# Optimization experiments

Hardware: AMD Instinct MI355X
Metric: run time of the kernel (lower is better)

## Reference

```python
import jax, jax.numpy as jnp
import numpy as np

H = 16          # hidden_size
L = 24          # num_layers
LEN_TRAIN = 96
LEN_PRED = 48
B = 256         # leading dim of input (acts as TIME axis for the LSTMs, see notes)


def setup_inputs() -> dict:
    key = jax.random.key(0)
    ks = jax.random.split(key, 16)
    s = 1.0 / np.sqrt(H)  # PyTorch LSTM/Linear init scale
    u = lambda k, shp: jax.random.uniform(k, shp, jnp.float32, -s, s)
    return {
        "x": jax.random.normal(ks[0], (B, 1, LEN_TRAIN), jnp.float32),
        # lstm1: layer0 input_size=1, layers 1..23 input_size=2H
        "W_ih0_1": u(ks[1], (2, 4 * H, 1)),
        "W_ih_1": u(ks[2], (L - 1, 2, 4 * H, 2 * H)),
        "W_hh_1": u(ks[3], (L, 2, 4 * H, H)),
        "b_ih_1": u(ks[4], (L, 2, 4 * H)),
        "b_hh_1": u(ks[5], (L, 2, 4 * H)),
        # lstm2: all layers input_size=2H
        "W_ih_2": u(ks[6], (L, 2, 4 * H, 2 * H)),
        "W_hh_2": u(ks[7], (L, 2, 4 * H, H)),
        "b_ih_2": u(ks[8], (L, 2, 4 * H)),
        "b_hh_2": u(ks[9], (L, 2, 4 * H)),
        "fc1_w": u(ks[10], (1000, 2 * LEN_PRED * H)),
        "fc1_b": u(ks[11], (1000,)),
        "fc2_w": u(ks[12], (LEN_PRED, 1000)),
        "fc2_b": u(ks[13], (LEN_PRED,)),
    }


def _lstm_dir(x, Wih, Whh, bih, bhh, reverse):
    # x: (T, N, in). Precompute input-gate GEMM over whole sequence.
    xg = jnp.einsum("tni,gi->tng", x, Wih) + bih + bhh  # (T, N, 4H)

    def step(carry, g_in):
        h, c = carry
        g = g_in + h @ Whh.T
        i, f, gg, o = jnp.split(g, 4, axis=-1)  # PyTorch gate order i,f,g,o
        c = jax.nn.sigmoid(f) * c + jax.nn.sigmoid(i) * jnp.tanh(gg)
        h = jax.nn.sigmoid(o) * jnp.tanh(c)
        return (h, c), h

    N = x.shape[1]
    init = (jnp.zeros((N, H), x.dtype), jnp.zeros((N, H), x.dtype))
    _, hs = jax.lax.scan(step, init, xg, reverse=reverse)
    return hs  # (T, N, H), in original time order


def _bilstm_stack(x, Wih_per_layer, Whh, bih, bhh):
    for l in range(Whh.shape[0]):
        Wih = Wih_per_layer[l]
        fwd = _lstm_dir(x, Wih[0], Whh[l, 0], bih[l, 0], bhh[l, 0], False)
        bwd = _lstm_dir(x, Wih[1], Whh[l, 1], bih[l, 1], bhh[l, 1], True)
        x = jnp.concatenate([fwd, bwd], axis=-1)  # (T, N, 2H)
    return x


def reference(x, W_ih0_1, W_ih_1, W_hh_1, b_ih_1, b_hh_1,
              W_ih_2, W_hh_2, b_ih_2, b_hh_2,
              fc1_w, fc1_b, fc2_w, fc2_b):
    xp = jnp.transpose(x, (0, 2, 1))  # (B, 96, 1); dim0 is the LSTM time axis (batch_first=False quirk)
    wih1 = [W_ih0_1] + [W_ih_1[i] for i in range(L - 1)]
    h = _bilstm_stack(xp, wih1, W_hh_1, b_ih_1, b_hh_1)      # (B, 96, 2H)
    x1 = h[:, -LEN_PRED:, :]                                  # (B, 48, 2H)
    wih2 = [W_ih_2[i] for i in range(L)]
    h2 = _bilstm_stack(x1, wih2, W_hh_2, b_ih_2, b_hh_2)      # (B, 48, 2H)
    z = h2 + x1
    flat = z.reshape(z.shape[0], -1)                          # (B, 1536)
    y = jax.nn.relu(flat @ fc1_w.T + fc1_b) @ fc2_w.T + fc2_b # (B, 48)
    return jnp.transpose(y.reshape(y.shape[0], LEN_PRED, 1), (0, 2, 1))  # (B, 1, 48)
```

## Files before the change

### kernel.cpp

```cpp
#include <hip/hip_runtime.h>


template <int SEL>
__device__ __forceinline__ float quad_bcast(float v) {
  return __int_as_float(__builtin_amdgcn_update_dpp(
      0, __float_as_int(v), SEL * 0x55, 0xF, 0xF, true));
}

__global__ __launch_bounds__(512, 2) void lstm_fused(
    const float* __restrict__ x, const float* __restrict__ W_ih0_1,
    const float* __restrict__ W_ih_1, const float* __restrict__ W_hh_1,
    const float* __restrict__ b_ih_1, const float* __restrict__ b_hh_1,
    const float* __restrict__ W_ih_2, const float* __restrict__ W_hh_2,
    const float* __restrict__ b_ih_2, const float* __restrict__ b_hh_2,
    float* __restrict__ x1out, float* __restrict__ h2out) {
  __shared__ float xgF[256 * 64];
  __shared__ float xgB[256 * 64];

  const int tid = threadIdx.x;
  const int lane = tid & 63;
  const int w = tid >> 6;
  const int np = blockIdx.x;
  const int nglob = 48 + np;

  const bool rec = (w == 0) || (w == 5);
  const int d = (w == 5) ? 1 : 0;
  const bool ovl = (w == 2) || (w == 3) || (w == 6) || (w == 7);
  const int ovlIdx = (w & 1) | ((w >> 2) << 1);
  const int widx = (w < 5) ? (w - 1) : (w - 2);

  {
    const int dd = w >> 2;
    const int wv = w & 3;
    float* xg = dd ? xgB : xgF;
    const float bias = b_ih_1[dd * 64 + lane] + b_hh_1[dd * 64 + lane];
    const float wih0 = W_ih0_1[dd * 64 + lane];
    const int xvb = __float_as_int(x[(size_t)(wv * 64 + lane) * 96 + nglob]);
    for (int ti = 0; ti < 64; ++ti) {
      const float xs = __int_as_float(__builtin_amdgcn_readlane(xvb, ti));
      xg[(wv * 64 + ti) * 64 + lane] = fmaf(wih0, xs, bias);
    }
  }

  int g = 0, r = 0;
  float s_ = 0.f, m_ = 0.f, b_ = 0.f;
  float whn[16];
  if (rec) {
    g = lane & 3;
    r = g * 16 + (lane >> 2);
    s_ = (g == 2) ? 2.885390082f : -1.442695041f;
    m_ = (g == 2) ? -2.0f : 1.0f;
    b_ = (g == 2) ? 1.0f : 0.0f;
    const float* W0 = W_hh_1 + (size_t)d * 1024 + (size_t)r * 16;
#pragma unroll
    for (int k = 0; k < 16; ++k) whn[k] = W0[k];
  }
  __syncthreads();

  for (int L = 0; L < 48; ++L) {
    float whh[16];
    if (rec) {
#pragma unroll
      for (int k = 0; k < 16; ++k) whh[k] = whn[k];
      const int M = (L < 47) ? (L + 1) : 47;
      const float* Wn = ((M < 24) ? (W_hh_1 + (size_t)M * 2048)
                                  : (W_hh_2 + (size_t)(M - 24) * 2048)) +
                        (size_t)d * 1024 + (size_t)r * 16;
#pragma unroll
      for (int k = 0; k < 16; ++k) whn[k] = Wn[k];
    }

    float wf[32], wb[32], bf = 0.f, bb = 0.f;
    if (!rec) {
      const int M = (L < 47) ? (L + 1) : 47;
      const float* WihP;
      const float* bihP;
      const float* bhhP;
      if (M < 24) {
        WihP = W_ih_1 + (size_t)(M - 1) * 4096;
        bihP = b_ih_1 + (size_t)M * 128;
        bhhP = b_hh_1 + (size_t)M * 128;
      } else {
        WihP = W_ih_2 + (size_t)(M - 24) * 4096;
        bihP = b_ih_2 + (size_t)(M - 24) * 128;
        bhhP = b_hh_2 + (size_t)(M - 24) * 128;
      }
      bf = bihP[lane] + bhhP[lane];
      bb = bihP[64 + lane] + bhhP[64 + lane];
      const float4* pf =
          reinterpret_cast<const float4*>(WihP + (size_t)lane * 32);
      const float4* pb =
          reinterpret_cast<const float4*>(WihP + 2048 + (size_t)lane * 32);
#pragma unroll
      for (int q = 0; q < 8; ++q) {
        const float4 a = pf[q];
        wf[4 * q + 0] = a.x;
        wf[4 * q + 1] = a.y;
        wf[4 * q + 2] = a.z;
        wf[4 * q + 3] = a.w;
        const float4 b = pb[q];
        wb[4 * q + 0] = b.x;
        wb[4 * q + 1] = b.y;
        wb[4 * q + 2] = b.z;
        wb[4 * q + 3] = b.w;
      }
    }

    auto compute_row = [&](int t, const float4 (&F)[4], const float4 (&Bv)[4]) {
      float f0 = bf, f1 = 0.f, f2 = 0.f, f3 = 0.f;
      float g0 = bb, g1 = 0.f, g2 = 0.f, g3 = 0.f;
#pragma unroll
      for (int q = 0; q < 4; ++q) {
        const float4 a = F[q];
        f0 = fmaf(wf[4 * q + 0], a.x, f0);
        f1 = fmaf(wf[4 * q + 1], a.y, f1);
        f2 = fmaf(wf[4 * q + 2], a.z, f2);
        f3 = fmaf(wf[4 * q + 3], a.w, f3);
        g0 = fmaf(wb[4 * q + 0], a.x, g0);
        g1 = fmaf(wb[4 * q + 1], a.y, g1);
        g2 = fmaf(wb[4 * q + 2], a.z, g2);
        g3 = fmaf(wb[4 * q + 3], a.w, g3);
        const float4 b = Bv[q];
        f0 = fmaf(wf[16 + 4 * q + 0], b.x, f0);
        f1 = fmaf(wf[16 + 4 * q + 1], b.y, f1);
        f2 = fmaf(wf[16 + 4 * q + 2], b.z, f2);
        f3 = fmaf(wf[16 + 4 * q + 3], b.w, f3);
        g0 = fmaf(wb[16 + 4 * q + 0], b.x, g0);
        g1 = fmaf(wb[16 + 4 * q + 1], b.y, g1);
        g2 = fmaf(wb[16 + 4 * q + 2], b.z, g2);
        g3 = fmaf(wb[16 + 4 * q + 3], b.w, g3);
      }
      xgF[t * 64 + lane] = (f0 + f1) + (f2 + f3);
      xgB[t * 64 + lane] = (g0 + g1) + (g2 + g3);
    };

    auto phaseA_rows = [&](int t0, int cnt) {
      float4 af[4], ab4[4], nf[4], nb[4];
      {
        const float4* qf = reinterpret_cast<const float4*>(&xgF[t0 * 64]);
        const float4* qb = reinterpret_cast<const float4*>(&xgB[t0 * 64]);
#pragma unroll
        for (int q = 0; q < 4; ++q) {
          af[q] = qf[q];
          ab4[q] = qb[q];
        }
      }
      for (int i = 0; i < cnt; i += 2) {
        const int t = t0 + i;
        {
          const float4* qf =
              reinterpret_cast<const float4*>(&xgF[(t + 1) * 64]);
          const float4* qb =
              reinterpret_cast<const float4*>(&xgB[(t + 1) * 64]);
#pragma unroll
          for (int q = 0; q < 4; ++q) {
            nf[q] = qf[q];
            nb[q] = qb[q];
          }
        }
        compute_row(t, af, ab4);
        if (i + 2 < cnt) {
          const float4* qf =
              reinterpret_cast<const float4*>(&xgF[(t + 2) * 64]);
          const float4* qb =
              reinterpret_cast<const float4*>(&xgB[(t + 2) * 64]);
#pragma unroll
          for (int q = 0; q < 4; ++q) {
            af[q] = qf[q];
            ab4[q] = qb[q];
          }
        }
        compute_row(t + 1, nf, nb);
      }
    };

    float hs[16];
    float c = 0.f;
    int t = d ? 255 : 0;
    const int dt = d ? -1 : 1;
    float cur0 = 0.f, cur1 = 0.f;
    float* xg = d ? xgB : xgF;

#define LSTM_STEP(CUR, TT)                                                  \
  {                                                                         \
    float a0 = (CUR), a1 = 0.f, a2 = 0.f, a3 = 0.f;                         \
    _Pragma("unroll") for (int k = 0; k < 16; k += 4) {                     \
      a0 = fmaf(whh[k + 0], hs[k + 0], a0);                                 \
      a1 = fmaf(whh[k + 1], hs[k + 1], a1);                                 \
      a2 = fmaf(whh[k + 2], hs[k + 2], a2);                                 \
      a3 = fmaf(whh[k + 3], hs[k + 3], a3);                                 \
    }                                                                       \
    const float gv = (a0 + a1) + (a2 + a3);                                 \
    const float e = __builtin_amdgcn_exp2f(s_ * gv);                        \
    const float v = fmaf(m_, __builtin_amdgcn_rcpf(1.0f + e), b_);          \
    const float si = quad_bcast<0>(v);                                      \
    const float sf = quad_bcast<1>(v);                                      \
    const float tg = quad_bcast<2>(v);                                      \
    const float so = quad_bcast<3>(v);                                      \
    c = fmaf(sf, c, si * tg);                                               \
    const float e2 = __builtin_amdgcn_exp2f(2.885390082f * c);              \
    const float th = fmaf(-2.0f, __builtin_amdgcn_rcpf(1.0f + e2), 1.0f);   \
    const float h = so * th;                                                \
    xg[(TT)*64 + r] = h;  \
    const int hb = __float_as_int(h);                                       \
    _Pragma("unroll") for (int k = 0; k < 16; ++k) hs[k] =                  \
        __int_as_float(__builtin_amdgcn_readlane(hb, 4 * k));               \
  }

    auto run_steps = [&](int nsteps) {
      for (int tt = 0; tt < nsteps; tt += 2) {
        const float nx0 = xg[((t + 2 * dt) & 255) * 64 + r];
        LSTM_STEP(cur0, t)
        const float nx1 = xg[((t + 3 * dt) & 255) * 64 + r];
        LSTM_STEP(cur1, t + dt)
        cur0 = nx0;
        cur1 = nx1;
        t += 2 * dt;
      }
    };

    if (rec) {
#pragma unroll
      for (int k = 0; k < 16; ++k) hs[k] = 0.f;
      cur0 = xg[t * 64 + r];
      cur1 = xg[(t + dt) * 64 + r];
      run_steps(192);
    }
    __syncthreads();

    if (rec) {
      __builtin_amdgcn_s_setprio(1);
      run_steps(64);
      __builtin_amdgcn_s_setprio(0);
    } else if (ovl && L != 23 && L != 47) {
      phaseA_rows(64 + ovlIdx * 32, 32);
    }
#undef LSTM_STEP
    __syncthreads();

    if (L == 23 || L == 47) {
      float* dst = (L == 23) ? x1out : h2out;
#pragma unroll
      for (int p = 0; p < 4; ++p) {
        const int gi = p * 512 + tid;
        const int tt = gi >> 3;
        const int cc = gi & 7;
        const float* src =
            (cc < 4) ? &xgF[tt * 64 + cc * 4] : &xgB[tt * 64 + (cc - 4) * 4];
        const float4 v = *reinterpret_cast<const float4*>(src);
        *reinterpret_cast<float4*>(dst + ((size_t)tt * 48 + np) * 32 +
                                   cc * 4) = v;
      }
      if (L == 47) break;
      __syncthreads();
      if (!rec) {
        const int t0 = (widx < 4) ? widx * 44 : 176 + (widx - 4) * 40;
        phaseA_rows(t0, (widx < 4) ? 44 : 40);
      }
    } else {
      if (!rec) {
        const int half = widx / 3;
        const int k3 = widx - half * 3;
        phaseA_rows(half * 192 + k3 * 22, (k3 == 2) ? 20 : 22);
      }
    }
    __syncthreads();
  }
}

__global__ __launch_bounds__(256) void fc1_kernel(
    const float* __restrict__ h2, const float* __restrict__ x1b,
    const float* __restrict__ w1, const float* __restrict__ b1,
    float* __restrict__ y1) {
  __shared__ float Zs[16][68];
  __shared__ float Ws[16][68];
  const int tid = threadIdx.x;
  const int m0 = blockIdx.x * 64;
  const int b0 = blockIdx.y * 64;
  const int rr = tid >> 2;
  const int c4 = (tid & 3) * 4;
  const int tx = tid & 15, ty = tid >> 4;

  float acc[4][4];
#pragma unroll
  for (int i = 0; i < 4; ++i)
#pragma unroll
    for (int jj = 0; jj < 4; ++jj) acc[i][jj] = 0.f;

  const bool wvalid = (m0 + rr) < 1000;
  const float* zr = h2 + (size_t)(b0 + rr) * 1536 + c4;
  const float* zr2 = x1b + (size_t)(b0 + rr) * 1536 + c4;
  const float* wr = w1 + (size_t)(m0 + rr) * 1536 + c4;

  float4 za = *reinterpret_cast<const float4*>(zr);
  float4 zb = *reinterpret_cast<const float4*>(zr2);
  float4 wv = wvalid ? *reinterpret_cast<const float4*>(wr)
                     : make_float4(0.f, 0.f, 0.f, 0.f);

  for (int k0 = 0; k0 < 1536; k0 += 16) {
    Zs[c4 + 0][rr] = za.x + zb.x;
    Zs[c4 + 1][rr] = za.y + zb.y;
    Zs[c4 + 2][rr] = za.z + zb.z;
    Zs[c4 + 3][rr] = za.w + zb.w;
    Ws[c4 + 0][rr] = wv.x;
    Ws[c4 + 1][rr] = wv.y;
    Ws[c4 + 2][rr] = wv.z;
    Ws[c4 + 3][rr] = wv.w;
    if (k0 + 16 < 1536) {
      za = *reinterpret_cast<const float4*>(zr + k0 + 16);
      zb = *reinterpret_cast<const float4*>(zr2 + k0 + 16);
      if (wvalid) wv = *reinterpret_cast<const float4*>(wr + k0 + 16);
    }
    __syncthreads();
#pragma unroll
    for (int kk = 0; kk < 16; ++kk) {
      const float4 av = *reinterpret_cast<const float4*>(&Zs[kk][ty * 4]);
      const float4 bv = *reinterpret_cast<const float4*>(&Ws[kk][tx * 4]);
      const float a_[4] = {av.x, av.y, av.z, av.w};
      const float b_[4] = {bv.x, bv.y, bv.z, bv.w};
#pragma unroll
      for (int i = 0; i < 4; ++i)
#pragma unroll
        for (int jj = 0; jj < 4; ++jj)
          acc[i][jj] = fmaf(a_[i], b_[jj], acc[i][jj]);
    }
    __syncthreads();
  }
#pragma unroll
  for (int i = 0; i < 4; ++i) {
    const int b = b0 + ty * 4 + i;
#pragma unroll
    for (int jj = 0; jj < 4; ++jj) {
      const int m = m0 + tx * 4 + jj;
      if (m < 1000) {
        float vo = acc[i][jj] + b1[m];
        y1[(size_t)b * 1000 + m] = vo > 0.f ? vo : 0.f;
      }
    }
  }
}

__global__ __launch_bounds__(64) void fc2_kernel(
    const float* __restrict__ y1, const float* __restrict__ w2,
    const float* __restrict__ b2, float* __restrict__ out) {
  __shared__ float ys[1000];
  const int b = blockIdx.x;
  for (int k = threadIdx.x; k < 1000; k += 64) ys[k] = y1[(size_t)b * 1000 + k];
  __syncthreads();
  const int p = threadIdx.x;
  if (p < 48) {
    float a0 = b2[p], a1 = 0.f, a2 = 0.f, a3 = 0.f;
    const float* wr = w2 + (size_t)p * 1000;
    for (int k = 0; k < 1000; k += 4) {
      const float4 wv = *reinterpret_cast<const float4*>(wr + k);
      a0 = fmaf(ys[k + 0], wv.x, a0);
      a1 = fmaf(ys[k + 1], wv.y, a1);
      a2 = fmaf(ys[k + 2], wv.z, a2);
      a3 = fmaf(ys[k + 3], wv.w, a3);
    }
    out[(size_t)b * 48 + p] = (a0 + a1) + (a2 + a3);
  }
}

extern "C" void kernel_launch(void* const* d_in, const int* in_sizes, int n_in,
                              void* d_out, int out_size, void* d_ws,
                              size_t ws_size, hipStream_t stream) {
  const float* x = (const float*)d_in[0];
  const float* W_ih0_1 = (const float*)d_in[1];
  const float* W_ih_1 = (const float*)d_in[2];
  const float* W_hh_1 = (const float*)d_in[3];
  const float* b_ih_1 = (const float*)d_in[4];
  const float* b_hh_1 = (const float*)d_in[5];
  const float* W_ih_2 = (const float*)d_in[6];
  const float* W_hh_2 = (const float*)d_in[7];
  const float* b_ih_2 = (const float*)d_in[8];
  const float* b_hh_2 = (const float*)d_in[9];
  const float* fc1_w = (const float*)d_in[10];
  const float* fc1_b = (const float*)d_in[11];
  const float* fc2_w = (const float*)d_in[12];
  const float* fc2_b = (const float*)d_in[13];

  float* ws = (float*)d_ws;
  float* x1b = ws;
  float* h2b = ws + 393216;
  float* y1 = ws + 786432;

  lstm_fused<<<48, 512, 0, stream>>>(x, W_ih0_1, W_ih_1, W_hh_1, b_ih_1,
                                     b_hh_1, W_ih_2, W_hh_2, b_ih_2, b_hh_2,
                                     x1b, h2b);
  fc1_kernel<<<dim3(16, 4), 256, 0, stream>>>(h2b, x1b, fc1_w, fc1_b, y1);
  fc2_kernel<<<256, 64, 0, stream>>>(y1, fc2_w, fc2_b, (float*)d_out);
}
```

Before: 2.422 ms.

## Split recurrent tail into two overlap phases and shrink post-layer input-projection work

The last 64 recurrence steps are split into two barrier-separated phases. The non-recurrent warps compute more of the next layer's input-gate projection while the recurrence is still running, which leaves a smaller serial projection chunk after each layer. The recurrence loop is rewritten with a pointer that steps by a constant stride, replacing the masked index arithmetic, and forward and backward paths are specialised. Launch bounds drop to one block per CU, which loosens register limits but may reduce occupancy. The extra barrier and the more intricate row partitioning add risk of mistakes in the row coverage.

```diff
diff --git a/kernel.cpp b/kernel.cpp
--- a/kernel.cpp
+++ b/kernel.cpp
@@ -7,7 +7,7 @@
       0, __float_as_int(v), SEL * 0x55, 0xF, 0xF, true));
 }
 
-__global__ __launch_bounds__(512, 2) void lstm_fused(
+__global__ __launch_bounds__(512, 1) void lstm_fused(
     const float* __restrict__ x, const float* __restrict__ W_ih0_1,
     const float* __restrict__ W_ih_1, const float* __restrict__ W_hh_1,
     const float* __restrict__ b_ih_1, const float* __restrict__ b_hh_1,
@@ -58,6 +58,8 @@
   __syncthreads();
 
   for (int L = 0; L < 48; ++L) {
+    const bool wo = (L == 23) || (L == 47);
+
     float whh[16];
     if (rec) {
 #pragma unroll
@@ -176,69 +178,125 @@
 
     float hs[16];
     float c = 0.f;
-    int t = d ? 255 : 0;
-    const int dt = d ? -1 : 1;
     float cur0 = 0.f, cur1 = 0.f;
-    float* xg = d ? xgB : xgF;
-
-#define LSTM_STEP(CUR, TT)                                                  \
-  {                                                                         \
-    float a0 = (CUR), a1 = 0.f, a2 = 0.f, a3 = 0.f;                         \
-    _Pragma("unroll") for (int k = 0; k < 16; k += 4) {                     \
-      a0 = fmaf(whh[k + 0], hs[k + 0], a0);                                 \
-      a1 = fmaf(whh[k + 1], hs[k + 1], a1);                                 \
-      a2 = fmaf(whh[k + 2], hs[k + 2], a2);                                 \
-      a3 = fmaf(whh[k + 3], hs[k + 3], a3);                                 \
-    }                                                                       \
-    const float gv = (a0 + a1) + (a2 + a3);                                 \
-    const float e = __builtin_amdgcn_exp2f(s_ * gv);                        \
-    const float v = fmaf(m_, __builtin_amdgcn_rcpf(1.0f + e), b_);          \
-    const float si = quad_bcast<0>(v);                                      \
-    const float sf = quad_bcast<1>(v);                                      \
-    const float tg = quad_bcast<2>(v);                                      \
-    const float so = quad_bcast<3>(v);                                      \
-    c = fmaf(sf, c, si * tg);                                               \
-    const float e2 = __builtin_amdgcn_exp2f(2.885390082f * c);              \
-    const float th = fmaf(-2.0f, __builtin_amdgcn_rcpf(1.0f + e2), 1.0f);   \
-    const float h = so * th;                                                \
-    xg[(TT)*64 + r] = h;  \
-    const int hb = __float_as_int(h);                                       \
-    _Pragma("unroll") for (int k = 0; k < 16; ++k) hs[k] =                  \
-        __int_as_float(__builtin_amdgcn_readlane(hb, 4 * k));               \
-  }
-
-    auto run_steps = [&](int nsteps) {
-      for (int tt = 0; tt < nsteps; tt += 2) {
-        const float nx0 = xg[((t + 2 * dt) & 255) * 64 + r];
-        LSTM_STEP(cur0, t)
-        const float nx1 = xg[((t + 3 * dt) & 255) * 64 + r];
-        LSTM_STEP(cur1, t + dt)
+    float* ap = nullptr;
+
+#define LSTM_CORE(CUR, HVAR)                                              \
+  {                                                                       \
+    float a0 = (CUR), a1 = 0.f, a2 = 0.f, a3 = 0.f;                       \
+    _Pragma("unroll") for (int k = 0; k < 16; k += 4) {                   \
+      a0 = fmaf(whh[k + 0], hs[k + 0], a0);                               \
+      a1 = fmaf(whh[k + 1], hs[k + 1], a1);                               \
+      a2 = fmaf(whh[k + 2], hs[k + 2], a2);                               \
+      a3 = fmaf(whh[k + 3], hs[k + 3], a3);                               \
+    }                                                                     \
+    const float gv = (a0 + a1) + (a2 + a3);                               \
+    const float e = __builtin_amdgcn_exp2f(s_ * gv);                      \
+    const float v = fmaf(m_, __builtin_amdgcn_rcpf(1.0f + e), b_);        \
+    const float si = quad_bcast<0>(v);                                    \
+    const float sf = quad_bcast<1>(v);                                    \
+    const float tg = quad_bcast<2>(v);                                    \
+    const float so = quad_bcast<3>(v);                                    \
+    c = fmaf(sf, c, si * tg);                                             \
+    const float e2 = __builtin_amdgcn_exp2f(2.885390082f * c);            \
+    const float th = fmaf(-2.0f, __builtin_amdgcn_rcpf(1.0f + e2), 1.0f); \
+    HVAR = so * th;                                                       \
+    const int hb = __float_as_int(HVAR);                                  \
+    _Pragma("unroll") for (int k = 0; k < 16; ++k) hs[k] =                \
+        __int_as_float(__builtin_amdgcn_readlane(hb, 4 * k));             \
+  }
+
+    auto fwd_run = [&](int iters) {
+      for (int it = 0; it < iters; ++it) {
+        const float nx0 = ap[128];
+        const float nx1 = ap[192];
+        float h0, h1;
+        LSTM_CORE(cur0, h0)
+        LSTM_CORE(cur1, h1)
+        ap[0] = h0;
+        ap[64] = h1;
         cur0 = nx0;
         cur1 = nx1;
-        t += 2 * dt;
+        ap += 128;
       }
     };
-
-    if (rec) {
+    auto bwd_run = [&](int iters) {
+      for (int it = 0; it < iters; ++it) {
+        const float nx1 = ap[0];
+        const float nx0 = ap[64];
+        float h0, h1;
+        LSTM_CORE(cur0, h0)
+        LSTM_CORE(cur1, h1)
+        ap[192] = h0;
+        ap[128] = h1;
+        cur0 = nx0;
+        cur1 = nx1;
+        ap -= 128;
+      }
+    };
+
+    if (w == 0) {
 #pragma unroll
       for (int k = 0; k < 16; ++k) hs[k] = 0.f;
-      cur0 = xg[t * 64 + r];
-      cur1 = xg[(t + dt) * 64 + r];
-      run_steps(192);
-    }
-    __syncthreads();
-
-    if (rec) {
+      c = 0.f;
+      ap = &xgF[r];
+      cur0 = ap[0];
+      cur1 = ap[64];
+      fwd_run(96);
+    } else if (w == 5) {
+#pragma unroll
+      for (int k = 0; k < 16; ++k) hs[k] = 0.f;
+      c = 0.f;
+      ap = &xgB[252 * 64 + r];
+      cur0 = ap[192];
+      cur1 = ap[128];
+      bwd_run(96);
+    }
+    __syncthreads();
+
+    if (w == 0) {
       __builtin_amdgcn_s_setprio(1);
-      run_steps(64);
+      fwd_run(16);
       __builtin_amdgcn_s_setprio(0);
-    } else if (ovl && L != 23 && L != 47) {
-      phaseA_rows(64 + ovlIdx * 32, 32);
-    }
-#undef LSTM_STEP
-    __syncthreads();
-
-    if (L == 23 || L == 47) {
+    } else if (w == 5) {
+      __builtin_amdgcn_s_setprio(1);
+      bwd_run(16);
+      __builtin_amdgcn_s_setprio(0);
+    } else if (ovl && !wo) {
+      phaseA_rows(64 + 32 * ovlIdx, 32);
+    }
+    __syncthreads();
+
+    if (w == 0) {
+      __builtin_amdgcn_s_setprio(1);
+      fwd_run(15);
+      {
+        float h0, h1;
+        LSTM_CORE(cur0, h0)
+        LSTM_CORE(cur1, h1)
+        ap[0] = h0;
+        ap[64] = h1;
+      }
+      __builtin_amdgcn_s_setprio(0);
+    } else if (w == 5) {
+      __builtin_amdgcn_s_setprio(1);
+      bwd_run(15);
+      {
+        float h0, h1;
+        LSTM_CORE(cur0, h0)
+        LSTM_CORE(cur1, h1)
+        ap[192] = h0;
+        ap[128] = h1;
+      }
+      __builtin_amdgcn_s_setprio(0);
+    } else if (ovl && !wo) {
+      phaseA_rows((ovlIdx < 2) ? (32 + 16 * ovlIdx) : (192 + 16 * (ovlIdx - 2)),
+                  16);
+    }
+#undef LSTM_CORE
+    __syncthreads();
+
+    if (wo) {
       float* dst = (L == 23) ? x1out : h2out;
 #pragma unroll
       for (int p = 0; p < 4; ++p) {
@@ -259,9 +317,15 @@
       }
     } else {
       if (!rec) {
-        const int half = widx / 3;
-        const int k3 = widx - half * 3;
-        phaseA_rows(half * 192 + k3 * 22, (k3 == 2) ? 20 : 22);
+        int t0, cnt;
+        if (widx < 3) {
+          t0 = (widx == 0) ? 0 : (2 + 10 * widx);
+          cnt = (widx == 0) ? 12 : 10;
+        } else {
+          t0 = 224 + ((widx == 3) ? 0 : (2 + 10 * (widx - 3)));
+          cnt = (widx == 3) ? 12 : 10;
+        }
+        phaseA_rows(t0, cnt);
       }
     }
     __syncthreads();
```

Result: slower. 2.476 ms (+2.2%).

## Run forward and backward LSTM recurrences interleaved in a single wavefront

Applied to the files above, without the earlier changes.

Replaces the two recurrent wavefronts (one per direction) with a single wavefront that advances forward and backward chains together, interleaving their FMAs, transcendental ops and broadcasts to hide latency. The next-layer input projection work is redistributed across the remaining seven wavefronts in three phases, and launch bounds drop to one block per CU. Weight prefetching of the next layer's W_hh is removed. This frees one wavefront for projection work at the cost of a longer dependent instruction stream in the recurrent wavefront and lower occupancy.

```diff
diff --git a/kernel.cpp b/kernel.cpp
--- a/kernel.cpp
+++ b/kernel.cpp
@@ -7,7 +7,7 @@
       0, __float_as_int(v), SEL * 0x55, 0xF, 0xF, true));
 }
 
-__global__ __launch_bounds__(512, 2) void lstm_fused(
+__global__ __launch_bounds__(512, 1) void lstm_fused(
     const float* __restrict__ x, const float* __restrict__ W_ih0_1,
     const float* __restrict__ W_ih_1, const float* __restrict__ W_hh_1,
     const float* __restrict__ b_ih_1, const float* __restrict__ b_hh_1,
@@ -23,11 +23,7 @@
   const int np = blockIdx.x;
   const int nglob = 48 + np;
 
-  const bool rec = (w == 0) || (w == 5);
-  const int d = (w == 5) ? 1 : 0;
-  const bool ovl = (w == 2) || (w == 3) || (w == 6) || (w == 7);
-  const int ovlIdx = (w & 1) | ((w >> 2) << 1);
-  const int widx = (w < 5) ? (w - 1) : (w - 2);
+  const bool rec = (w == 0);
 
   {
     const int dd = w >> 2;
@@ -44,30 +40,27 @@
 
   int g = 0, r = 0;
   float s_ = 0.f, m_ = 0.f, b_ = 0.f;
-  float whn[16];
   if (rec) {
     g = lane & 3;
     r = g * 16 + (lane >> 2);
     s_ = (g == 2) ? 2.885390082f : -1.442695041f;
     m_ = (g == 2) ? -2.0f : 1.0f;
     b_ = (g == 2) ? 1.0f : 0.0f;
-    const float* W0 = W_hh_1 + (size_t)d * 1024 + (size_t)r * 16;
-#pragma unroll
-    for (int k = 0; k < 16; ++k) whn[k] = W0[k];
   }
   __syncthreads();
 
   for (int L = 0; L < 48; ++L) {
-    float whh[16];
+    const bool wo = (L == 23) || (L == 47);
+
+    float whF[16], whB[16];
     if (rec) {
-#pragma unroll
-      for (int k = 0; k < 16; ++k) whh[k] = whn[k];
-      const int M = (L < 47) ? (L + 1) : 47;
-      const float* Wn = ((M < 24) ? (W_hh_1 + (size_t)M * 2048)
-                                  : (W_hh_2 + (size_t)(M - 24) * 2048)) +
-                        (size_t)d * 1024 + (size_t)r * 16;
-#pragma unroll
-      for (int k = 0; k < 16; ++k) whn[k] = Wn[k];
+      const float* Wl = ((L < 24) ? (W_hh_1 + (size_t)L * 2048)
+                                  : (W_hh_2 + (size_t)(L - 24) * 2048)) +
+                        (size_t)r * 16;
+#pragma unroll
+      for (int k = 0; k < 16; ++k) whF[k] = Wl[k];
+#pragma unroll
+      for (int k = 0; k < 16; ++k) whB[k] = Wl[1024 + k];
     }
 
     float wf[32], wb[32], bf = 0.f, bb = 0.f;
@@ -174,71 +167,102 @@
       }
     };
 
-    float hs[16];
-    float c = 0.f;
-    int t = d ? 255 : 0;
-    const int dt = d ? -1 : 1;
-    float cur0 = 0.f, cur1 = 0.f;
-    float* xg = d ? xgB : xgF;
-
-#define LSTM_STEP(CUR, TT)                                                  \
-  {                                                                         \
-    float a0 = (CUR), a1 = 0.f, a2 = 0.f, a3 = 0.f;                         \
-    _Pragma("unroll") for (int k = 0; k < 16; k += 4) {                     \
-      a0 = fmaf(whh[k + 0], hs[k + 0], a0);                                 \
-      a1 = fmaf(whh[k + 1], hs[k + 1], a1);                                 \
-      a2 = fmaf(whh[k + 2], hs[k + 2], a2);                                 \
-      a3 = fmaf(whh[k + 3], hs[k + 3], a3);                                 \
-    }                                                                       \
-    const float gv = (a0 + a1) + (a2 + a3);                                 \
-    const float e = __builtin_amdgcn_exp2f(s_ * gv);                        \
-    const float v = fmaf(m_, __builtin_amdgcn_rcpf(1.0f + e), b_);          \
-    const float si = quad_bcast<0>(v);                                      \
-    const float sf = quad_bcast<1>(v);                                      \
-    const float tg = quad_bcast<2>(v);                                      \
-    const float so = quad_bcast<3>(v);                                      \
-    c = fmaf(sf, c, si * tg);                                               \
-    const float e2 = __builtin_amdgcn_exp2f(2.885390082f * c);              \
-    const float th = fmaf(-2.0f, __builtin_amdgcn_rcpf(1.0f + e2), 1.0f);   \
-    const float h = so * th;                                                \
-    xg[(TT)*64 + r] = h;  \
-    const int hb = __float_as_int(h);                                       \
-    _Pragma("unroll") for (int k = 0; k < 16; ++k) hs[k] =                  \
-        __int_as_float(__builtin_amdgcn_readlane(hb, 4 * k));               \
-  }
-
-    auto run_steps = [&](int nsteps) {
-      for (int tt = 0; tt < nsteps; tt += 2) {
-        const float nx0 = xg[((t + 2 * dt) & 255) * 64 + r];
-        LSTM_STEP(cur0, t)
-        const float nx1 = xg[((t + 3 * dt) & 255) * 64 + r];
-        LSTM_STEP(cur1, t + dt)
-        cur0 = nx0;
-        cur1 = nx1;
-        t += 2 * dt;
-      }
-    };
+    float hsF[16], hsB[16];
+    float cF = 0.f, cB = 0.f;
+    float curF = 0.f, curB = 0.f;
+    float* apF = nullptr;
+    float* apB = nullptr;
+
+#define PAIR_STEP                                                         \
+  {                                                                       \
+    const float nxF = apF[64];     \
+    const float nxB = apB[-64];                       \
+    float fa0 = curF, fa1 = 0.f, fa2 = 0.f, fa3 = 0.f;                    \
+    float ba0 = curB, ba1 = 0.f, ba2 = 0.f, ba3 = 0.f;                    \
+    _Pragma("unroll") for (int k = 0; k < 16; k += 4) {                   \
+      fa0 = fmaf(whF[k + 0], hsF[k + 0], fa0);                            \
+      ba0 = fmaf(whB[k + 0], hsB[k + 0], ba0);                            \
+      fa1 = fmaf(whF[k + 1], hsF[k + 1], fa1);                            \
+      ba1 = fmaf(whB[k + 1], hsB[k + 1], ba1);                            \
+      fa2 = fmaf(whF[k + 2], hsF[k + 2], fa2);                            \
+      ba2 = fmaf(whB[k + 2], hsB[k + 2], ba2);                            \
+      fa3 = fmaf(whF[k + 3], hsF[k + 3], fa3);                            \
+      ba3 = fmaf(whB[k + 3], hsB[k + 3], ba3);                            \
+    }                                                                     \
+    const float gvF = (fa0 + fa1) + (fa2 + fa3);                          \
+    const float gvB = (ba0 + ba1) + (ba2 + ba3);                          \
+    const float eF = __builtin_amdgcn_exp2f(s_ * gvF);                    \
+    const float eB = __builtin_amdgcn_exp2f(s_ * gvB);                    \
+    const float vF = fmaf(m_, __builtin_amdgcn_rcpf(1.0f + eF), b_);      \
+    const float vB = fmaf(m_, __builtin_amdgcn_rcpf(1.0f + eB), b_);      \
+    const float siF = quad_bcast<0>(vF);                                  \
+    const float siB = quad_bcast<0>(vB);                                  \
+    const float sfF = quad_bcast<1>(vF);                                  \
+    const float sfB = quad_bcast<1>(vB);                                  \
+    const float tgF = quad_bcast<2>(vF);                                  \
+    const float tgB = quad_bcast<2>(vB);                                  \
+    const float soF = quad_bcast<3>(vF);                                  \
+    const float soB = quad_bcast<3>(vB);                                  \
+    cF = fmaf(sfF, cF, siF * tgF);                                        \
+    cB = fmaf(sfB, cB, siB * tgB);                                        \
+    const float e2F = __builtin_amdgcn_exp2f(2.885390082f * cF);          \
+    const float e2B = __builtin_amdgcn_exp2f(2.885390082f * cB);          \
+    const float thF = fmaf(-2.0f, __builtin_amdgcn_rcpf(1.0f + e2F), 1.0f); \
+    const float thB = fmaf(-2.0f, __builtin_amdgcn_rcpf(1.0f + e2B), 1.0f); \
+    const float hF = soF * thF;                                           \
+    const float hB = soB * thB;                                           \
+    apF[0] = hF;           \
+    apB[0] = hB;                                                          \
+    const int hbF = __float_as_int(hF);                                   \
+    const int hbB = __float_as_int(hB);                                   \
+    _Pragma("unroll") for (int k = 0; k < 16; ++k) {                      \
+      hsF[k] = __int_as_float(__builtin_amdgcn_readlane(hbF, 4 * k));     \
+      hsB[k] = __int_as_float(__builtin_amdgcn_readlane(hbB, 4 * k));     \
+    }                                                                     \
+    curF = nxF;                                                           \
+    curB = nxB;                                                           \
+    apF += 64;                                                            \
+    apB -= 64;                                                            \
+  }
 
     if (rec) {
 #pragma unroll
-      for (int k = 0; k < 16; ++k) hs[k] = 0.f;
-      cur0 = xg[t * 64 + r];
-      cur1 = xg[(t + dt) * 64 + r];
-      run_steps(192);
+      for (int k = 0; k < 16; ++k) {
+        hsF[k] = 0.f;
+        hsB[k] = 0.f;
+      }
+      cF = 0.f;
+      cB = 0.f;
+      apF = &xgF[r];
+      apB = &xgB[255 * 64 + r];
+      curF = apF[0];
+      curB = apB[0];
+      for (int it = 0; it < 192; ++it) PAIR_STEP
     }
     __syncthreads();
 
     if (rec) {
-      __builtin_amdgcn_s_setprio(1);
-      run_steps(64);
-      __builtin_amdgcn_s_setprio(0);
-    } else if (ovl && L != 23 && L != 47) {
-      phaseA_rows(64 + ovlIdx * 32, 32);
-    }
-#undef LSTM_STEP
-    __syncthreads();
-
-    if (L == 23 || L == 47) {
+      for (int it = 0; it < 32; ++it) PAIR_STEP
+    } else if (w != 4 && !wo) {
+      const int widx6 = (w < 4) ? (w - 1) : (w - 2);
+      const int t0 =
+          64 + ((widx6 < 4) ? 22 * widx6 : 88 + 20 * (widx6 - 4));
+      phaseA_rows(t0, (widx6 < 4) ? 22 : 20);
+    }
+    __syncthreads();
+
+    if (rec) {
+      for (int it = 0; it < 32; ++it) PAIR_STEP
+    } else if (w != 4 && !wo) {
+      const int k3 = (w < 4) ? (w - 1) : (w - 5);
+      const int base = (w < 4) ? 32 : 192;
+      phaseA_rows(base + ((k3 == 0) ? 0 : (12 + 10 * (k3 - 1))),
+                  (k3 == 0) ? 12 : 10);
+    }
+#undef PAIR_STEP
+    __syncthreads();
+
+    if (wo) {
       float* dst = (L == 23) ? x1out : h2out;
 #pragma unroll
       for (int p = 0; p < 4; ++p) {
@@ -254,14 +278,25 @@
       if (L == 47) break;
       __syncthreads();
       if (!rec) {
-        const int t0 = (widx < 4) ? widx * 44 : 176 + (widx - 4) * 40;
-        phaseA_rows(t0, (widx < 4) ? 44 : 40);
+        int t0, cnt;
+        if (w <= 4) {
+          t0 = 38 * (w - 1);
+          cnt = 38;
+        } else if (w == 5) {
+          t0 = 152;
+          cnt = 36;
+        } else {
+          t0 = 188 + 34 * (w - 6);
+          cnt = 34;
+        }
+        phaseA_rows(t0, cnt);
       }
     } else {
-      if (!rec) {
-        const int half = widx / 3;
-        const int k3 = widx - half * 3;
-        phaseA_rows(half * 192 + k3 * 22, (k3 == 2) ? 20 : 22);
+      if (!rec && w != 4) {
+        const int k3 = (w < 4) ? (w - 1) : (w - 5);
+        const int base = (w < 4) ? 0 : 224;
+        phaseA_rows(base + ((k3 == 0) ? 0 : (12 + 10 * (k3 - 1))),
+                    (k3 == 0) ? 12 : 10);
       }
     }
     __syncthreads();
```

Result: slower. 3.804 ms (+57.0%).
